# Kernel optimization log

Measured on AMD Instinct MI355X. Metric: run time of the kernel, lower is better.

Reference implementation:

```python
import jax, jax.numpy as jnp
import numpy as np

HEADS = 4
AGENT = 49  # 7x7 agent tokens
LN_EPS = 1e-5


def setup_inputs() -> dict:
    key = jax.random.key(0)
    ks = jax.random.split(key, 3)
    B, C, H, W = 2, 128, 56, 56
    x = jax.random.normal(ks[0], (B, C, H, W), jnp.float32)
    # 1x1 convs == per-pixel linear maps; store as [out_ch, in_ch]
    w_qkv = jax.random.normal(ks[1], (3 * C, C), jnp.float32) * (C ** -0.5)
    w_proj = jax.random.normal(ks[2], (C, C), jnp.float32) * (C ** -0.5)
    b_proj = jnp.zeros((C,), jnp.float32)
    ln_g = jnp.ones((C,), jnp.float32)
    ln_b = jnp.zeros((C,), jnp.float32)
    return {"x": x, "w_qkv": w_qkv, "w_proj": w_proj, "b_proj": b_proj,
            "ln_g": ln_g, "ln_b": ln_b}


def reference(x, w_qkv, w_proj, b_proj, ln_g, ln_b):
    B, C, H, W = x.shape
    heads = HEADS
    hd = C // heads
    N = H * W
    scale = hd ** -0.5
    a = int(AGENT ** 0.5)  # 7; H,W divisible by a -> exact adaptive avg pool

    # 1x1-conv QKV: [B,3C,H,W] -> [B,3,heads,hd,N] -> q,k,v [B,h,N,hd]
    qkv = jnp.einsum('oc,bchw->bohw', w_qkv, x).reshape(B, 3, heads, hd, N)
    q = jnp.transpose(qkv[:, 0], (0, 1, 3, 2))
    k = jnp.transpose(qkv[:, 1], (0, 1, 3, 2))
    v = jnp.transpose(qkv[:, 2], (0, 1, 3, 2))

    # agent tokens: adaptive avg pool to (a,a) == uniform block mean
    agent = x.reshape(B, C, a, H // a, a, W // a).mean(axis=(3, 5))  # [B,C,a,a]
    agent = agent.reshape(B, heads, hd, AGENT)
    agent = jnp.transpose(agent, (0, 1, 3, 2))  # [B,h,A,hd]

    # stage 1: compress q through agent tokens
    q_to_agent = jax.nn.softmax(
        jnp.einsum('bhnd,bhad->bhna', q * scale, agent), axis=-1)  # [B,h,N,A]
    q_compressed = jnp.einsum('bhna,bhad->bhnd', q_to_agent, agent)  # [B,h,N,hd]

    # stage 2: full N x N attention with compressed queries
    attn = jax.nn.softmax(
        jnp.einsum('bhnd,bhmd->bhnm', q_compressed * scale, k), axis=-1)
    out = jnp.einsum('bhnm,bhmd->bhnd', attn, v)  # [B,h,N,hd]

    # merge heads -> [B,N,C], 1x1-conv proj, LayerNorm over C
    out = jnp.transpose(out, (0, 2, 1, 3)).reshape(B, N, C)
    out = jnp.einsum('bnc,oc->bno', out, w_proj) + b_proj
    mu = out.mean(-1, keepdims=True)
    var = out.var(-1, keepdims=True)
    out = (out - mu) / jnp.sqrt(var + LN_EPS) * ln_g + ln_b
    return jnp.transpose(out.reshape(B, H, W, C), (0, 3, 1, 2))
```

## Files before the change

kernel.cpp:

```cpp
#include <hip/hip_runtime.h>
#include <hip/hip_bf16.h>
#include <stdint.h>

typedef unsigned short u16;
typedef __attribute__((ext_vector_type(8))) short short8;
typedef __attribute__((ext_vector_type(4))) short short4v;
typedef __attribute__((ext_vector_type(4))) float f32x4;

#define NB 2
#define NC 128
#define NHD 4
#define HD 32
#define NN 3136
#define NA 49
#define NSPLIT 4
#define NKP 3200
#define NTILE 25
#define SCALE 0.17677669529663687f
#define LOG2E 1.4426950408889634f
#define QSC (SCALE * LOG2E)

__device__ inline u16 bfb(float f) {
    __hip_bfloat16 h = __float2bfloat16(f);
    return *(u16*)&h;
}
__device__ inline float b2f(u16 w) {
    return __uint_as_float(((uint32_t)w) << 16);
}
__device__ inline short4v pack4(float a, float b, float c, float d) {
    union { short4v s; __hip_bfloat162 h[2]; } u;
    u.h[0] = __float22bfloat162_rn(make_float2(a, b));
    u.h[1] = __float22bfloat162_rn(make_float2(c, d));
    return u.s;
}
__device__ inline float ldf(const void* p, size_t i, int f) {
    return f ? b2f(((const u16*)p)[i]) : ((const float*)p)[i];
}
__device__ inline void gld16(const u16* g, u16* l) {
    __builtin_amdgcn_global_load_lds(
        (__attribute__((address_space(1))) void*)(g),
        (__attribute__((address_space(3))) void*)(l), 16, 0, 0);
}
__device__ inline void stage8k(const u16* g, u16* lds, int w, int lane) {
    gld16(g + (size_t)(w * 64 + lane) * 8,       lds + (size_t)w * 512);
    gld16(g + (size_t)(256 + w * 64 + lane) * 8, lds + 2048 + (size_t)w * 512);
}
__device__ inline int detect_local(const u16* raw, int t) {
    __shared__ int cnt;
    if (t == 0) cnt = 0;
    __syncthreads();
    float a = fabsf(b2f(raw[t * 97]));
    if (a >= 1e-4f && a <= 100.0f) atomicAdd(&cnt, 1);
    __syncthreads();
    return cnt >= 230;
}

__global__ __launch_bounds__(256) void k_prep(const void* __restrict__ xr,
                                              const void* __restrict__ wq,
                                              const void* __restrict__ wp,
                                              const void* __restrict__ bp,
                                              const void* __restrict__ g,
                                              const void* __restrict__ bb,
                                              u16* __restrict__ xT,
                                              u16* __restrict__ wbf,
                                              u16* __restrict__ wpb,
                                              float* __restrict__ bgb,
                                              u16* __restrict__ agb,
                                              u16* __restrict__ agT,
                                              int* __restrict__ flagOut) {
    __shared__ u16 tile[128][18];
    int bx = blockIdx.x, t = threadIdx.x;
    int f = detect_local((const u16*)xr, t);
    if (bx < 392) {
        int b = bx / 196;
        int n0 = (bx % 196) * 16;
        int c = t >> 1, nh = (t & 1) * 8;
        size_t src = ((size_t)(b * 128 + c)) * NN + n0 + nh;
#pragma unroll
        for (int i = 0; i < 8; ++i) tile[c][nh + i] = bfb(ldf(xr, src + i, f));
        __syncthreads();
        int n = t >> 4, c0 = (t & 15) * 8;
        short8 o;
#pragma unroll
        for (int i = 0; i < 8; ++i) o[i] = (short)tile[c0 + i][n];
        *(short8*)&xT[((size_t)b * NN + n0 + n) * 128 + c0] = o;
    } else if (bx < 584) {
        int i = (bx - 392) * 256 + t;
        wbf[i] = bfb(ldf(wq, i, f));
    } else if (bx < 648) {
        int i = (bx - 584) * 256 + t;
        wpb[i] = bfb(ldf(wp, i, f));
    } else if (bx < 650) {
        int i = (bx - 648) * 256 + t;
        if (i < 128)      bgb[i] = ldf(bp, i, f);
        else if (i < 256) bgb[i] = ldf(g, i - 128, f);
        else if (i < 384) bgb[i] = ldf(bb, i - 256, f);
        if (bx == 648 && t == 0) *flagOut = f;
    } else {
        int idx = (bx - 650) * 256 + t;
        const int NPOOL = NB * NC * NA;
        if (idx < NPOOL) {
            int b = idx / (NC * NA);
            int r = idx % (NC * NA);
            int c = r / NA;
            int a = r % NA;
            int ai = a / 7, aj = a % 7;
            size_t base = ((size_t)(b * NC + c)) * NN + ai * 8 * 56 + aj * 8;
            float s = 0.f;
            if (f) {
                const u16* xp = (const u16*)xr + base;
#pragma unroll
                for (int uu = 0; uu < 8; ++uu) {
                    ushort4 a0 = *(const ushort4*)&xp[uu * 56];
                    ushort4 a1 = *(const ushort4*)&xp[uu * 56 + 4];
                    s += b2f(a0.x) + b2f(a0.y) + b2f(a0.z) + b2f(a0.w)
                       + b2f(a1.x) + b2f(a1.y) + b2f(a1.z) + b2f(a1.w);
                }
            } else {
                const float* xp = (const float*)xr + base;
#pragma unroll
                for (int uu = 0; uu < 8; ++uu) {
                    float4 v0 = *(const float4*)&xp[uu * 56];
                    float4 v1 = *(const float4*)&xp[uu * 56 + 4];
                    s += v0.x + v0.y + v0.z + v0.w + v1.x + v1.y + v1.z + v1.w;
                }
            }
            int h = c >> 5, d = c & 31;
            int bh = b * NHD + h;
            u16 val = bfb(s * (1.f / 64.f));
            agb[bh * 2048 + a * 32 + d] = val;
            agT[bh * 2048 + d * 64 + a] = val;
        } else {
            int j = idx - NPOOL;
            if (j < 3840) {
                int bh = j / 480, rem = j % 480;
                int a = 49 + rem / 32, d = rem % 32;
                agb[bh * 2048 + a * 32 + d] = 0;
            } else if (j < 7680) {
                j -= 3840;
                int bh = j / 480, rem = j % 480;
                int a = 49 + rem / 32, d = rem % 32;
                agT[bh * 2048 + d * 64 + a] = 0;
            }
        }
    }
}

__global__ __launch_bounds__(256, 4) void k_qkv_s1(const u16* __restrict__ xT,
                                                   const u16* __restrict__ wbf,
                                                   const u16* __restrict__ agb,
                                                   const u16* __restrict__ agT,
                                                   u16* __restrict__ kbf,
                                                   u16* __restrict__ vtb,
                                                   u16* __restrict__ qcb) {
    __shared__ u16 qtile[2 * 64 * 40];
    int b = blockIdx.z;
    int n0 = blockIdx.x * 64;
    int w = threadIdx.x >> 6, lane = threadIdx.x & 63;
    int c = lane & 15, u = lane >> 4;
    int o0 = blockIdx.y * 64 + w * 16;
    const f32x4 z = {0.f, 0.f, 0.f, 0.f};
    short8 af0 = *(const short8*)&wbf[(o0 + c) * 128 +  0 + u * 8];
    short8 af1 = *(const short8*)&wbf[(o0 + c) * 128 + 32 + u * 8];
    short8 af2 = *(const short8*)&wbf[(o0 + c) * 128 + 64 + u * 8];
    short8 af3 = *(const short8*)&wbf[(o0 + c) * 128 + 96 + u * 8];
    int tq = o0 >> 7, h = (o0 >> 5) & 3, d0 = (o0 & 31) + u * 4;
    size_t bh = (size_t)b * NHD + h;
    const u16* xb = &xT[(size_t)b * NN * 128];
#pragma unroll
    for (int nt = 0; nt < 4; ++nt) {
        int n = n0 + nt * 16 + c;
        f32x4 acc = z;
        acc = __builtin_amdgcn_mfma_f32_16x16x32_bf16(af0,
            *(const short8*)&xb[(size_t)n * 128 +  0 + u * 8], acc, 0, 0, 0);
        acc = __builtin_amdgcn_mfma_f32_16x16x32_bf16(af1,
            *(const short8*)&xb[(size_t)n * 128 + 32 + u * 8], acc, 0, 0, 0);
        acc = __builtin_amdgcn_mfma_f32_16x16x32_bf16(af2,
            *(const short8*)&xb[(size_t)n * 128 + 64 + u * 8], acc, 0, 0, 0);
        acc = __builtin_amdgcn_mfma_f32_16x16x32_bf16(af3,
            *(const short8*)&xb[(size_t)n * 128 + 96 + u * 8], acc, 0, 0, 0);
        if (tq == 0) {
            int hl = (o0 >> 5) & 1;
            *(short4v*)&qtile[(hl * 64 + nt * 16 + c) * 40 + d0] =
                pack4(acc[0] * QSC, acc[1] * QSC, acc[2] * QSC, acc[3] * QSC);
        } else if (tq == 1) {
            *(short4v*)&kbf[(bh * NKP + n) * HD + d0] =
                pack4(acc[0], acc[1], acc[2], acc[3]);
        } else {
            int tile = n >> 7, kt2 = n & 127;
            int sub = kt2 >> 4, uu = (kt2 >> 2) & 3, jj = n & 3;
            size_t vb0 = ((size_t)bh * NTILE + tile) * 4096 + sub * 512 + uu * 128 + jj;
#pragma unroll
            for (int r = 0; r < 4; ++r)
                vtb[vb0 + (d0 + r) * 4] = bfb(acc[r]);
        }
    }
    if (blockIdx.y < 2) {
        __syncthreads();
#pragma unroll
        for (int tt = w; tt < 8; tt += 4) {
            int hl2 = tt >> 2, r0 = (tt & 3) * 16;
            int hg = blockIdx.y * 2 + hl2;
            size_t bh2 = (size_t)b * NHD + hg;
            const u16* aB = agb + bh2 * 2048;
            const u16* aT = agT + bh2 * 2048;
            short8 qf = *(const short8*)&qtile[(hl2 * 64 + r0 + c) * 40 + u * 8];
            f32x4 st[4];
#pragma unroll
            for (int t2 = 0; t2 < 4; ++t2) {
                short8 afr = *(const short8*)&aB[(t2 * 16 + c) * 32 + u * 8];
                st[t2] = __builtin_amdgcn_mfma_f32_16x16x32_bf16(afr, qf, z, 0, 0, 0);
            }
            float e[4][4];
            float lsum = 0.f;
#pragma unroll
            for (int t2 = 0; t2 < 4; ++t2)
#pragma unroll
                for (int r = 0; r < 4; ++r) {
                    float v = __builtin_amdgcn_exp2f(st[t2][r]);
                    if (t2 == 3 && !(u == 0 && r == 0)) v = 0.f;
                    e[t2][r] = v;
                    lsum += v;
                }
            lsum += __shfl_xor(lsum, 16);
            lsum += __shfl_xor(lsum, 32);
            float linv = 1.f / lsum;
            f32x4 qlo = z, qhi = z;
#pragma unroll
            for (int t2 = 0; t2 < 4; ++t2) {
                short4v pf = pack4(e[t2][0] * linv, e[t2][1] * linv,
                                   e[t2][2] * linv, e[t2][3] * linv);
                short4v alo = *(const short4v*)&aT[c * 64 + t2 * 16 + u * 4];
                short4v ahi = *(const short4v*)&aT[(c + 16) * 64 + t2 * 16 + u * 4];
                qlo = __builtin_amdgcn_mfma_f32_16x16x16bf16_1k(alo, pf, qlo, 0, 0, 0);
                qhi = __builtin_amdgcn_mfma_f32_16x16x16bf16_1k(ahi, pf, qhi, 0, 0, 0);
            }
            u16* dst = &qcb[(bh2 * NN + n0 + r0 + c) * HD];
            *(short4v*)&dst[u * 4]      = pack4(qlo[0] * QSC, qlo[1] * QSC, qlo[2] * QSC, qlo[3] * QSC);
            *(short4v*)&dst[16 + u * 4] = pack4(qhi[0] * QSC, qhi[1] * QSC, qhi[2] * QSC, qhi[3] * QSC);
        }
    }
}

__global__ __launch_bounds__(256, 3) void k_flash4(const u16* __restrict__ qc,
                                                   const u16* __restrict__ kb,
                                                   const u16* __restrict__ vt,
                                                   u16* __restrict__ opb,
                                                   float* __restrict__ lp) {
    __shared__ __align__(16) u16 Ks[2][4096];
    __shared__ __align__(16) u16 Vs[2][4096];
    int b = blockIdx.z;
    int h = blockIdx.y & 3;
    int s = blockIdx.y >> 2;
    int w = threadIdx.x >> 6, lane = threadIdx.x & 63;
    int c = lane & 15, u = lane >> 4;
    int qa = blockIdx.x * 128 + w * 32;
    int qbr = qa + 16;
    if (qa  > NN - 16) qa  = NN - 16;
    if (qbr > NN - 16) qbr = NN - 16;
    size_t bh = (size_t)b * NHD + h;
    const u16* kg = kb + bh * (size_t)NKP * HD;
    const u16* vg = vt + bh * (size_t)NTILE * 4096;
    short8 qfA = *(const short8*)(qc + (bh * NN + qa  + c) * HD + u * 8);
    short8 qfB = *(const short8*)(qc + (bh * NN + qbr + c) * HD + u * 8);
    const f32x4 z = {0.f, 0.f, 0.f, 0.f};
    f32x4 oA0 = z, oA1 = z, oB0 = z, oB1 = z;
    float lA = 0.f, lB = 0.f;
    int t0 = (s * NTILE) / NSPLIT, t1 = ((s + 1) * NTILE) / NSPLIT;
    stage8k(kg + (size_t)t0 * 4096, &Ks[0][0], w, lane);
    stage8k(vg + (size_t)t0 * 4096, &Vs[0][0], w, lane);
#pragma unroll 1
    for (int t = t0; t < t1; ++t) {
        int buf = (t - t0) & 1;
        __syncthreads();
        if (t + 1 < t1) {
            stage8k(kg + (size_t)(t + 1) * 4096, &Ks[buf ^ 1][0], w, lane);
            stage8k(vg + (size_t)(t + 1) * 4096, &Vs[buf ^ 1][0], w, lane);
        }
        const u16* kp = &Ks[buf][0];
        const u16* vp = &Vs[buf][0];
        int kk = t * 128;
        bool tail = (kk + 128 > NN);
#pragma unroll
        for (int sub = 0; sub < 8; ++sub) {
            short8 kf = *(const short8*)(kp + sub * 512 + c * 32 + u * 8);
            f32x4 sA = __builtin_amdgcn_mfma_f32_16x16x32_bf16(kf, qfA, z, 0, 0, 0);
            f32x4 sB = __builtin_amdgcn_mfma_f32_16x16x32_bf16(kf, qfB, z, 0, 0, 0);
            float eA[4], eB[4];
#pragma unroll
            for (int r = 0; r < 4; ++r) {
                eA[r] = __builtin_amdgcn_exp2f(sA[r]);
                eB[r] = __builtin_amdgcn_exp2f(sB[r]);
            }
            if (tail) {
#pragma unroll
                for (int r = 0; r < 4; ++r)
                    if (kk + sub * 16 + u * 4 + r >= NN) { eA[r] = 0.f; eB[r] = 0.f; }
            }
            lA += (eA[0] + eA[1]) + (eA[2] + eA[3]);
            lB += (eB[0] + eB[1]) + (eB[2] + eB[3]);
            short4v pA = pack4(eA[0], eA[1], eA[2], eA[3]);
            short4v pB = pack4(eB[0], eB[1], eB[2], eB[3]);
            short4v va = *(const short4v*)(vp + sub * 512 + u * 128 + c * 4);
            short4v vb = *(const short4v*)(vp + sub * 512 + u * 128 + (c + 16) * 4);
            oA0 = __builtin_amdgcn_mfma_f32_16x16x16bf16_1k(va, pA, oA0, 0, 0, 0);
            oA1 = __builtin_amdgcn_mfma_f32_16x16x16bf16_1k(vb, pA, oA1, 0, 0, 0);
            oB0 = __builtin_amdgcn_mfma_f32_16x16x16bf16_1k(va, pB, oB0, 0, 0, 0);
            oB1 = __builtin_amdgcn_mfma_f32_16x16x16bf16_1k(vb, pB, oB1, 0, 0, 0);
        }
    }
    lA += __shfl_xor(lA, 16); lA += __shfl_xor(lA, 32);
    lB += __shfl_xor(lB, 16); lB += __shfl_xor(lB, 32);
    float iA = 1.f / lA, iB = 1.f / lB;
    u16* oba = opb + (((size_t)(s * NB + b)) * NN + qa + c) * NC + h * HD;
    *(short4v*)&oba[u * 4]      = pack4(oA0[0] * iA, oA0[1] * iA, oA0[2] * iA, oA0[3] * iA);
    *(short4v*)&oba[16 + u * 4] = pack4(oA1[0] * iA, oA1[1] * iA, oA1[2] * iA, oA1[3] * iA);
    u16* obb = opb + (((size_t)(s * NB + b)) * NN + qbr + c) * NC + h * HD;
    *(short4v*)&obb[u * 4]      = pack4(oB0[0] * iB, oB0[1] * iB, oB0[2] * iB, oB0[3] * iB);
    *(short4v*)&obb[16 + u * 4] = pack4(oB1[0] * iB, oB1[1] * iB, oB1[2] * iB, oB1[3] * iB);
    if (u == 0) {
        lp[(((size_t)(s * NB + b)) * NHD + h) * NN + qa  + c] = lA;
        lp[(((size_t)(s * NB + b)) * NHD + h) * NN + qbr + c] = lB;
    }
}

__global__ __launch_bounds__(256, 4) void k_proj2(const u16* __restrict__ opb,
                                                  const float* __restrict__ lp,
                                                  const u16* __restrict__ wpb,
                                                  const float* __restrict__ bgb,
                                                  void* __restrict__ out,
                                                  const int* __restrict__ flag) {
    __shared__ u16 Af[16 * 136];
    __shared__ float red1[4][16], red2[4][16];
    int bx = blockIdx.x;
    int b = bx >= 196;
    int n0 = (bx - b * 196) * 16;
    int t = threadIdx.x;
    {
        int row = t >> 4, c8 = (t & 15) * 8;
        int n = n0 + row;
        int hh = c8 >> 5;
        float num[8] = {};
        float den = 0.f;
#pragma unroll
        for (int s = 0; s < NSPLIT; ++s) {
            float ls = lp[(((size_t)(s * NB + b)) * NHD + hh) * NN + n];
            short8 o8 = *(const short8*)&opb[(((size_t)(s * NB + b)) * NN + n) * NC + c8];
            den += ls;
#pragma unroll
            for (int i = 0; i < 8; ++i) num[i] += ls * b2f((u16)o8[i]);
        }
        float inv = 1.f / den;
        u16* dst = &Af[row * 136 + c8];
#pragma unroll
        for (int i = 0; i < 8; i += 2) {
            __hip_bfloat162 p = __float22bfloat162_rn(
                make_float2(num[i] * inv, num[i + 1] * inv));
            *(uint32_t*)&dst[i] = *(uint32_t*)&p;
        }
    }
    __syncthreads();
    int w = t >> 6, lane = t & 63, c = lane & 15, u = lane >> 4;
    int oA = w * 32 + c, oB = w * 32 + 16 + c;
    const f32x4 z = {0.f, 0.f, 0.f, 0.f};
    f32x4 cA = z, cB = z;
#pragma unroll
    for (int kf = 0; kf < 4; ++kf) {
        short8 a  = *(const short8*)&Af[c * 136 + kf * 32 + u * 8];
        short8 bA = *(const short8*)&wpb[(size_t)oA * 128 + kf * 32 + u * 8];
        short8 bB = *(const short8*)&wpb[(size_t)oB * 128 + kf * 32 + u * 8];
        cA = __builtin_amdgcn_mfma_f32_16x16x32_bf16(a, bA, cA, 0, 0, 0);
        cB = __builtin_amdgcn_mfma_f32_16x16x32_bf16(a, bB, cB, 0, 0, 0);
    }
    float bpA = bgb[oA], bpB = bgb[oB];
    float s1[4], s2[4];
#pragma unroll
    for (int r = 0; r < 4; ++r) {
        cA[r] += bpA; cB[r] += bpB;
        s1[r] = cA[r] + cB[r];
        s2[r] = cA[r] * cA[r] + cB[r] * cB[r];
    }
#pragma unroll
    for (int off = 1; off < 16; off <<= 1)
#pragma unroll
        for (int r = 0; r < 4; ++r) {
            s1[r] += __shfl_xor(s1[r], off);
            s2[r] += __shfl_xor(s2[r], off);
        }
    if (c == 0)
#pragma unroll
        for (int r = 0; r < 4; ++r) {
            red1[w][u * 4 + r] = s1[r];
            red2[w][u * 4 + r] = s2[r];
        }
    __syncthreads();
    float gA = bgb[128 + oA], beA = bgb[256 + oA];
    float gB = bgb[128 + oB], beB = bgb[256 + oB];
    float outA[4], outB[4];
#pragma unroll
    for (int r = 0; r < 4; ++r) {
        int row = u * 4 + r;
        float S1 = (red1[0][row] + red1[1][row]) + (red1[2][row] + red1[3][row]);
        float S2 = (red2[0][row] + red2[1][row]) + (red2[2][row] + red2[3][row]);
        float mu = S1 * (1.f / NC);
        float ex = S2 * (1.f / NC);
        float rstd = rsqrtf(ex - mu * mu + 1e-5f);
        outA[r] = (cA[r] - mu) * rstd * gA + beA;
        outB[r] = (cB[r] - mu) * rstd * gB + beB;
    }
    int n = n0 + u * 4;
    if (*flag) {
        __hip_bfloat16* ob = (__hip_bfloat16*)out;
        ushort4 sA = make_ushort4(bfb(outA[0]), bfb(outA[1]), bfb(outA[2]), bfb(outA[3]));
        ushort4 sB = make_ushort4(bfb(outB[0]), bfb(outB[1]), bfb(outB[2]), bfb(outB[3]));
        *(ushort4*)&ob[((size_t)(b * NC + oA)) * NN + n] = sA;
        *(ushort4*)&ob[((size_t)(b * NC + oB)) * NN + n] = sB;
    } else {
        float* ob = (float*)out;
        *(float4*)&ob[((size_t)(b * NC + oA)) * NN + n] = make_float4(outA[0], outA[1], outA[2], outA[3]);
        *(float4*)&ob[((size_t)(b * NC + oB)) * NN + n] = make_float4(outB[0], outB[1], outB[2], outB[3]);
    }
}

extern "C" void kernel_launch(void* const* d_in, const int* in_sizes, int n_in,
                              void* d_out, int out_size, void* d_ws, size_t ws_size,
                              hipStream_t stream) {
    const void* x_raw  = d_in[0];
    const void* wq_raw = d_in[1];
    const void* wp_raw = d_in[2];
    const void* bp_raw = d_in[3];
    const void* lg_raw = d_in[4];
    const void* lb_raw = d_in[5];

    float* ws   = (float*)d_ws;
    int*   flag = (int*)d_ws;
    float* bgb  = ws + 16;
    float* lp   = bgb + 512;
    u16*   opb  = (u16*)(lp + (size_t)NSPLIT * NB * NHD * NN);
    u16*   xT   = opb + (size_t)NSPLIT * NB * NN * NC;
    u16*   wbf  = xT + (size_t)NB * NN * NC;
    u16*   wpb  = wbf + 3 * NC * NC;
    u16*   kbf  = wpb + NC * NC;
    u16*   vtb  = kbf + (size_t)NB * NHD * NKP * HD;
    u16*   qcb  = vtb + (size_t)NB * NHD * NTILE * 4096;
    u16*   agb  = qcb + (size_t)NB * NHD * NN * HD;
    u16*   agT  = agb + NB * NHD * 64 * 32;

    k_prep<<<729, 256, 0, stream>>>(x_raw, wq_raw, wp_raw, bp_raw, lg_raw, lb_raw,
                                    xT, wbf, wpb, bgb, agb, agT, flag);
    k_qkv_s1<<<dim3(NN / 64, 6, NB), 256, 0, stream>>>(xT, wbf, agb, agT,
                                                       kbf, vtb, qcb);
    k_flash4<<<dim3(25, NHD * NSPLIT, NB), 256, 0, stream>>>(qcb, kbf, vtb, opb, lp);
    k_proj2<<<392, 256, 0, stream>>>(opb, lp, wpb, bgb, d_out, flag);
}
```

Measured before the change: 119.3 us.

## Swizzle x, K and proj weights into MFMA-fragment tiles and stage via LDS

The transposed input, K buffer and projection weights are written in a tiled, fragment-ordered layout so each wave's MFMA operand loads become contiguous 16-byte chunks. The QKV kernel and the projection kernel copy their tile (x slab, full W_proj) into shared memory with direct global-to-LDS loads before the MMAs, and the flash kernel reads K in the new order. This targets strided, uncoalesced global reads of MFMA fragments, at the cost of extra LDS usage (which may lower occupancy) and a per-block copy of the whole projection weight. The K tail padding no longer has a separate region, so the flash kernel's tail-tile reads depend on the existing masking.

After: 115.5 us. 3.2% less time.

```diff
diff --git a/kernel.cpp b/kernel.cpp
--- a/kernel.cpp
+++ b/kernel.cpp
@@ -61,9 +61,9 @@
                                               const void* __restrict__ bp,
                                               const void* __restrict__ g,
                                               const void* __restrict__ bb,
-                                              u16* __restrict__ xT,
+                                              u16* __restrict__ xTs,
                                               u16* __restrict__ wbf,
-                                              u16* __restrict__ wpb,
+                                              u16* __restrict__ wps,
                                               float* __restrict__ bgb,
                                               u16* __restrict__ agb,
                                               u16* __restrict__ agT,
@@ -74,22 +74,26 @@
     if (bx < 392) {
         int b = bx / 196;
         int n0 = (bx % 196) * 16;
+        int T = n0 >> 6, nbase = n0 & 63;
         int c = t >> 1, nh = (t & 1) * 8;
         size_t src = ((size_t)(b * 128 + c)) * NN + n0 + nh;
 #pragma unroll
         for (int i = 0; i < 8; ++i) tile[c][nh + i] = bfb(ldf(xr, src + i, f));
         __syncthreads();
-        int n = t >> 4, c0 = (t & 15) * 8;
+        int n = t >> 4, ktu = t & 15;
+        int c0 = ktu * 8;
         short8 o;
 #pragma unroll
         for (int i = 0; i < 8; ++i) o[i] = (short)tile[c0 + i][n];
-        *(short8*)&xT[((size_t)b * NN + n0 + n) * 128 + c0] = o;
+        *(short8*)&xTs[(((size_t)b * 49 + T) * 16 + ktu) * 512 + (nbase + n) * 8] = o;
     } else if (bx < 584) {
         int i = (bx - 392) * 256 + t;
         wbf[i] = bfb(ldf(wq, i, f));
     } else if (bx < 648) {
         int i = (bx - 584) * 256 + t;
-        wpb[i] = bfb(ldf(wp, i, f));
+        int o = i >> 7, c = i & 127;
+        int otile = o >> 4, oloc = o & 15, ktu = c >> 3, wi = c & 7;
+        wps[((otile * 16 + ktu) * 16 + oloc) * 8 + wi] = bfb(ldf(wp, i, f));
     } else if (bx < 650) {
         int i = (bx - 648) * 256 + t;
         if (i < 128)      bgb[i] = ldf(bp, i, f);
@@ -146,18 +150,24 @@
     }
 }
 
-__global__ __launch_bounds__(256, 4) void k_qkv_s1(const u16* __restrict__ xT,
+__global__ __launch_bounds__(256, 4) void k_qkv_s1(const u16* __restrict__ xTs,
                                                    const u16* __restrict__ wbf,
                                                    const u16* __restrict__ agb,
                                                    const u16* __restrict__ agT,
                                                    u16* __restrict__ kbf,
                                                    u16* __restrict__ vtb,
                                                    u16* __restrict__ qcb) {
+    __shared__ __align__(16) u16 xs[8192];
     __shared__ u16 qtile[2 * 64 * 40];
     int b = blockIdx.z;
     int n0 = blockIdx.x * 64;
     int w = threadIdx.x >> 6, lane = threadIdx.x & 63;
     int c = lane & 15, u = lane >> 4;
+    int t = threadIdx.x;
+    const u16* xtile = xTs + (((size_t)b * 49 + (n0 >> 6)) * 16) * 512;
+#pragma unroll
+    for (int i = 0; i < 4; ++i)
+        gld16(xtile + (size_t)(i * 256 + t) * 8, xs + (size_t)(i * 256 + t) * 8);
     int o0 = blockIdx.y * 64 + w * 16;
     const f32x4 z = {0.f, 0.f, 0.f, 0.f};
     short8 af0 = *(const short8*)&wbf[(o0 + c) * 128 +  0 + u * 8];
@@ -166,25 +176,28 @@
     short8 af3 = *(const short8*)&wbf[(o0 + c) * 128 + 96 + u * 8];
     int tq = o0 >> 7, h = (o0 >> 5) & 3, d0 = (o0 & 31) + u * 4;
     size_t bh = (size_t)b * NHD + h;
-    const u16* xb = &xT[(size_t)b * NN * 128];
+    __syncthreads();
 #pragma unroll
     for (int nt = 0; nt < 4; ++nt) {
         int n = n0 + nt * 16 + c;
         f32x4 acc = z;
         acc = __builtin_amdgcn_mfma_f32_16x16x32_bf16(af0,
-            *(const short8*)&xb[(size_t)n * 128 +  0 + u * 8], acc, 0, 0, 0);
+            *(const short8*)&xs[((0 * 4 + u) * 64 + nt * 16 + c) * 8], acc, 0, 0, 0);
         acc = __builtin_amdgcn_mfma_f32_16x16x32_bf16(af1,
-            *(const short8*)&xb[(size_t)n * 128 + 32 + u * 8], acc, 0, 0, 0);
+            *(const short8*)&xs[((1 * 4 + u) * 64 + nt * 16 + c) * 8], acc, 0, 0, 0);
         acc = __builtin_amdgcn_mfma_f32_16x16x32_bf16(af2,
-            *(const short8*)&xb[(size_t)n * 128 + 64 + u * 8], acc, 0, 0, 0);
+            *(const short8*)&xs[((2 * 4 + u) * 64 + nt * 16 + c) * 8], acc, 0, 0, 0);
         acc = __builtin_amdgcn_mfma_f32_16x16x32_bf16(af3,
-            *(const short8*)&xb[(size_t)n * 128 + 96 + u * 8], acc, 0, 0, 0);
+            *(const short8*)&xs[((3 * 4 + u) * 64 + nt * 16 + c) * 8], acc, 0, 0, 0);
         if (tq == 0) {
             int hl = (o0 >> 5) & 1;
             *(short4v*)&qtile[(hl * 64 + nt * 16 + c) * 40 + d0] =
                 pack4(acc[0] * QSC, acc[1] * QSC, acc[2] * QSC, acc[3] * QSC);
         } else if (tq == 1) {
-            *(short4v*)&kbf[(bh * NKP + n) * HD + d0] =
+            int tile = n >> 7, sub = (n >> 4) & 7, key = n & 15;
+            int dg = d0 >> 3, wi = d0 & 7;
+            size_t kb0 = (((size_t)bh * NTILE + tile) * 8 + sub) * 4 + dg;
+            *(short4v*)&kbf[kb0 * 128 + key * 8 + wi] =
                 pack4(acc[0], acc[1], acc[2], acc[3]);
         } else {
             int tile = n >> 7, kt2 = n & 127;
@@ -259,7 +272,7 @@
     if (qa  > NN - 16) qa  = NN - 16;
     if (qbr > NN - 16) qbr = NN - 16;
     size_t bh = (size_t)b * NHD + h;
-    const u16* kg = kb + bh * (size_t)NKP * HD;
+    const u16* kg = kb + bh * (size_t)NTILE * 4096;
     const u16* vg = vt + bh * (size_t)NTILE * 4096;
     short8 qfA = *(const short8*)(qc + (bh * NN + qa  + c) * HD + u * 8);
     short8 qfB = *(const short8*)(qc + (bh * NN + qbr + c) * HD + u * 8);
@@ -283,7 +296,7 @@
         bool tail = (kk + 128 > NN);
 #pragma unroll
         for (int sub = 0; sub < 8; ++sub) {
-            short8 kf = *(const short8*)(kp + sub * 512 + c * 32 + u * 8);
+            short8 kf = *(const short8*)(kp + ((sub * 4 + u) * 16 + c) * 8);
             f32x4 sA = __builtin_amdgcn_mfma_f32_16x16x32_bf16(kf, qfA, z, 0, 0, 0);
             f32x4 sB = __builtin_amdgcn_mfma_f32_16x16x32_bf16(kf, qfB, z, 0, 0, 0);
             float eA[4], eB[4];
@@ -326,16 +339,20 @@
 
 __global__ __launch_bounds__(256, 4) void k_proj2(const u16* __restrict__ opb,
                                                   const float* __restrict__ lp,
-                                                  const u16* __restrict__ wpb,
+                                                  const u16* __restrict__ wps,
                                                   const float* __restrict__ bgb,
                                                   void* __restrict__ out,
                                                   const int* __restrict__ flag) {
+    __shared__ __align__(16) u16 wl[16384];
     __shared__ u16 Af[16 * 136];
     __shared__ float red1[4][16], red2[4][16];
     int bx = blockIdx.x;
     int b = bx >= 196;
     int n0 = (bx - b * 196) * 16;
     int t = threadIdx.x;
+#pragma unroll
+    for (int i = 0; i < 8; ++i)
+        gld16(wps + (size_t)(i * 256 + t) * 8, wl + (size_t)(i * 256 + t) * 8);
     {
         int row = t >> 4, c8 = (t & 15) * 8;
         int n = n0 + row;
@@ -367,8 +384,8 @@
 #pragma unroll
     for (int kf = 0; kf < 4; ++kf) {
         short8 a  = *(const short8*)&Af[c * 136 + kf * 32 + u * 8];
-        short8 bA = *(const short8*)&wpb[(size_t)oA * 128 + kf * 32 + u * 8];
-        short8 bB = *(const short8*)&wpb[(size_t)oB * 128 + kf * 32 + u * 8];
+        short8 bA = *(const short8*)&wl[(((2 * w) * 16 + kf * 4 + u) * 16 + c) * 8];
+        short8 bB = *(const short8*)&wl[(((2 * w + 1) * 16 + kf * 4 + u) * 16 + c) * 8];
         cA = __builtin_amdgcn_mfma_f32_16x16x32_bf16(a, bA, cA, 0, 0, 0);
         cB = __builtin_amdgcn_mfma_f32_16x16x32_bf16(a, bB, cB, 0, 0, 0);
     }
@@ -437,19 +454,19 @@
     float* bgb  = ws + 16;
     float* lp   = bgb + 512;
     u16*   opb  = (u16*)(lp + (size_t)NSPLIT * NB * NHD * NN);
-    u16*   xT   = opb + (size_t)NSPLIT * NB * NN * NC;
-    u16*   wbf  = xT + (size_t)NB * NN * NC;
-    u16*   wpb  = wbf + 3 * NC * NC;
-    u16*   kbf  = wpb + NC * NC;
-    u16*   vtb  = kbf + (size_t)NB * NHD * NKP * HD;
+    u16*   xTs  = opb + (size_t)NSPLIT * NB * NN * NC;
+    u16*   wbf  = xTs + (size_t)NB * NN * NC;
+    u16*   wps  = wbf + 3 * NC * NC;
+    u16*   kbf  = wps + NC * NC;
+    u16*   vtb  = kbf + (size_t)NB * NHD * NTILE * 4096;
     u16*   qcb  = vtb + (size_t)NB * NHD * NTILE * 4096;
     u16*   agb  = qcb + (size_t)NB * NHD * NN * HD;
     u16*   agT  = agb + NB * NHD * 64 * 32;
 
     k_prep<<<729, 256, 0, stream>>>(x_raw, wq_raw, wp_raw, bp_raw, lg_raw, lb_raw,
-                                    xT, wbf, wpb, bgb, agb, agT, flag);
-    k_qkv_s1<<<dim3(NN / 64, 6, NB), 256, 0, stream>>>(xT, wbf, agb, agT,
+                                    xTs, wbf, wps, bgb, agb, agT, flag);
+    k_qkv_s1<<<dim3(NN / 64, 6, NB), 256, 0, stream>>>(xTs, wbf, agb, agT,
                                                        kbf, vtb, qcb);
     k_flash4<<<dim3(25, NHD * NSPLIT, NB), 256, 0, stream>>>(qcb, kbf, vtb, opb, lp);
-    k_proj2<<<392, 256, 0, stream>>>(opb, lp, wpb, bgb, d_out, flag);
-}
+    k_proj2<<<392, 256, 0, stream>>>(opb, lp, wps, bgb, d_out, flag);
+}
```
